# Kernel tuning notes

Measured on AMD Instinct MI355X. Metric: run time of the kernel, lower is better.

The kernel has to match this reference:

```python
import jax, jax.numpy as jnp
import numpy as np

B, L, E = 2, 2048, 1024
NH, DH = 16, 64          # num_heads, attn_hidden_size
HID = 4096               # FFN hidden_size
EPS = 1e-5


def _layernorm(x, g, b):
    mu = jnp.mean(x, axis=-1, keepdims=True)
    var = jnp.var(x, axis=-1, keepdims=True)
    return (x - mu) * jax.lax.rsqrt(var + EPS) * g + b


def setup_inputs() -> dict:
    key = jax.random.key(0)
    ks = jax.random.split(key, 12)
    s = 0.02
    return {
        "x":    jax.random.normal(ks[0], (B, L, E), dtype=jnp.float32),
        "Wa":   jax.random.normal(ks[1], (E, NH * 3 * DH), dtype=jnp.float32) * s,
        "Wout": jax.random.normal(ks[2], (NH * DH, E), dtype=jnp.float32) * s,
        "bout": jnp.zeros((E,), dtype=jnp.float32),
        "W1":   jax.random.normal(ks[3], (E, HID), dtype=jnp.float32) * s,
        "b1":   jnp.zeros((HID,), dtype=jnp.float32),
        "W2":   jax.random.normal(ks[4], (HID, E), dtype=jnp.float32) * s,
        "b2":   jnp.zeros((E,), dtype=jnp.float32),
        "g1":   jnp.ones((E,), dtype=jnp.float32),
        "be1":  jnp.zeros((E,), dtype=jnp.float32),
        "g2":   jnp.ones((E,), dtype=jnp.float32),
        "be2":  jnp.zeros((E,), dtype=jnp.float32),
    }


def _attention(o, Wa, Wout, bout):
    b, l, e = o.shape
    tmp = o @ Wa                                   # (b, l, nh*3*dh)
    tmp = tmp.reshape(b, l, NH, 3 * DH).transpose(0, 2, 1, 3)  # (b, nh, l, 3dh)
    q, k, v = jnp.split(tmp, 3, axis=-1)           # each (b, nh, l, dh)
    scores = jnp.einsum('bhqd,bhkd->bhqk', q, k) / np.sqrt(DH)
    causal = jnp.tril(jnp.ones((l, l), dtype=bool))
    scores = jnp.where(causal, scores, -jnp.inf)
    A = jax.nn.softmax(scores, axis=-1)
    out = jnp.einsum('bhqk,bhkd->bhqd', A, v)      # (b, nh, l, dh)
    out = out.transpose(0, 2, 1, 3).reshape(b, l, NH * DH)
    return out @ Wout + bout


def reference(x, Wa, Wout, bout, W1, b1, W2, b2, g1, be1, g2, be2):
    o = _layernorm(x, g1, be1)
    o = _attention(o, Wa, Wout, bout)
    o = _layernorm(x + o, g2, be2)
    o = o @ W1 + b1          # activation is Identity
    o = x + (o @ W2 + b2)
    return o
```

## Files before the change

### kernel.cpp

```cpp
#include <hip/hip_runtime.h>
#include <hip/hip_bf16.h>

#define BB 2
#define LL 2048
#define EE 1024
#define NHH 16
#define DHH 64
#define HIDD 4096
#define MTOK (BB*LL)
#define NQKV (NHH*3*DHH)

typedef __attribute__((ext_vector_type(8))) short bf16x8;
typedef __attribute__((ext_vector_type(4))) float f32x4;

#define MFMA16(a,b,c) __builtin_amdgcn_mfma_f32_16x16x32_bf16(a,b,c,0,0,0)

static __device__ __forceinline__ void gload_lds16(const void* g, void* lds) {
  __builtin_amdgcn_global_load_lds(
      (const __attribute__((address_space(1))) unsigned int*)g,
      (__attribute__((address_space(3))) unsigned int*)lds, 16, 0, 0);
}

__global__ __launch_bounds__(256)
void convT_kernel(const float* __restrict__ W, __hip_bfloat16* __restrict__ WT,
                  int K, int N) {
  __shared__ float tile[32][33];
  const int tx = threadIdx.x & 31, ty = threadIdx.x >> 5;
  const int n0 = blockIdx.x * 32, k0 = blockIdx.y * 32;
#pragma unroll
  for (int i = 0; i < 4; ++i)
    tile[ty + i*8][tx] = W[(size_t)(k0 + ty + i*8) * N + n0 + tx];
  __syncthreads();
#pragma unroll
  for (int i = 0; i < 4; ++i)
    WT[(size_t)(n0 + ty + i*8) * K + k0 + tx] = __float2bfloat16(tile[tx][ty + i*8]);
}

__global__ __launch_bounds__(256)
void vtrans_kernel(const __hip_bfloat16* __restrict__ qkv,
                   __hip_bfloat16* __restrict__ VT) {
  __shared__ ushort tile[32][34];
  const int tx = threadIdx.x & 31, ty = threadIdx.x >> 5;
  const int tok0 = blockIdx.x * 32;
  const int dh0  = blockIdx.y * 32;
  const int bh   = blockIdx.z;
  const int b = bh >> 4, h = bh & 15;
  const ushort* src = (const ushort*)qkv;
#pragma unroll
  for (int i = 0; i < 4; ++i)
    tile[ty + i*8][tx] =
      src[(size_t)(b*LL + tok0 + ty + i*8) * NQKV + h*192 + 128 + dh0 + tx];
  __syncthreads();
  ushort* dst = (ushort*)VT;
#pragma unroll
  for (int i = 0; i < 4; ++i)
    dst[(size_t)(bh*DHH + dh0 + ty + i*8) * LL + tok0 + tx] = tile[tx][ty + i*8];
}

__global__ __launch_bounds__(256)
void ln_kernel(const float* __restrict__ in, const float* __restrict__ g,
               const float* __restrict__ be, __hip_bfloat16* __restrict__ out) {
  const int row = blockIdx.x;
  const int t = threadIdx.x;
  const float4 v = ((const float4*)(in + (size_t)row * EE))[t];
  float s = v.x + v.y + v.z + v.w;
  float q = v.x*v.x + v.y*v.y + v.z*v.z + v.w*v.w;
#pragma unroll
  for (int off = 32; off >= 1; off >>= 1) {
    s += __shfl_xor(s, off);
    q += __shfl_xor(q, off);
  }
  __shared__ float ps[4], pq[4];
  if ((t & 63) == 0) { ps[t >> 6] = s; pq[t >> 6] = q; }
  __syncthreads();
  s = ps[0] + ps[1] + ps[2] + ps[3];
  q = pq[0] + pq[1] + pq[2] + pq[3];
  const float mean = s * (1.0f / EE);
  const float rstd = rsqrtf(q * (1.0f / EE) - mean * mean + 1e-5f);
  const float4 gg = ((const float4*)g)[t];
  const float4 bb = ((const float4*)be)[t];
  union { ushort4 u; __hip_bfloat16 h[4]; } o;
  o.h[0] = __float2bfloat16((v.x - mean) * rstd * gg.x + bb.x);
  o.h[1] = __float2bfloat16((v.y - mean) * rstd * gg.y + bb.y);
  o.h[2] = __float2bfloat16((v.z - mean) * rstd * gg.z + bb.z);
  o.h[3] = __float2bfloat16((v.w - mean) * rstd * gg.w + bb.w);
  ((ushort4*)(out + (size_t)row * EE))[t] = o.u;
}

template<int BN, int OUT_BF16, int HAS_BIAS, int HAS_RES>
__device__ __forceinline__ void gemm_body(
    const __hip_bfloat16* __restrict__ A, const __hip_bfloat16* __restrict__ BT,
    void* __restrict__ Cv, const float* __restrict__ bias,
    const float* __restrict__ res, int M, int N, int K, int lda, int ldb) {
  constexpr int NF = BN / 32;
  __shared__ alignas(16) __hip_bfloat16 sA[2][128 * 32];
  __shared__ alignas(16) __hip_bfloat16 sB[2][BN * 32];
  const int t = threadIdx.x;
  const int wv = t >> 6, l = t & 63;
  const int lr = l & 15, lk = (l >> 4) * 8;

  const int nwg = gridDim.x * gridDim.y;
  int wg = blockIdx.y * gridDim.x + blockIdx.x;
  wg = (wg & 7) * (nwg >> 3) + (wg >> 3);
  const int bx = wg % gridDim.x, by = wg / gridDim.x;
  const int m0 = by * 128, n0 = bx * BN;

  const int wrow = (wv >> 1) * 64;
  const int wcol = (wv & 1) * (BN / 2);
  const int srow = t >> 2, scol = (t & 3) * 8;
  const __hip_bfloat16* gA = A + (size_t)(m0 + srow) * lda + scol;
  const __hip_bfloat16* gB = BT + (size_t)(n0 + srow) * ldb + scol;

  auto stage = [&](int buf, int k0) {
    char* dA = (char*)(&sA[buf][0]) + wv * 1024;
    gload_lds16(gA + k0, dA);
    gload_lds16(gA + (size_t)64 * lda + k0, dA + 4096);
    char* dB = (char*)(&sB[buf][0]) + wv * 1024;
    gload_lds16(gB + k0, dB);
    if constexpr (BN == 128)
      gload_lds16(gB + (size_t)64 * ldb + k0, dB + 4096);
  };

  f32x4 acc[4][NF] = {};

  auto compute = [&](int buf) {
    bf16x8 af[4], bfv[NF];
#pragma unroll
    for (int mi = 0; mi < 4; ++mi)
      af[mi] = *(const bf16x8*)(&sA[buf][(wrow + mi * 16 + lr) * 32 + lk]);
#pragma unroll
    for (int ni = 0; ni < NF; ++ni)
      bfv[ni] = *(const bf16x8*)(&sB[buf][(wcol + ni * 16 + lr) * 32 + lk]);
#pragma unroll
    for (int mi = 0; mi < 4; ++mi)
#pragma unroll
      for (int ni = 0; ni < NF; ++ni)
        acc[mi][ni] = MFMA16(af[mi], bfv[ni], acc[mi][ni]);
  };

  stage(0, 0);
  __syncthreads();
  for (int k0 = 0; k0 < K; k0 += 64) {
    stage(1, k0 + 32);
    compute(0);
    __syncthreads();
    if (k0 + 64 < K) stage(0, k0 + 64);
    compute(1);
    __syncthreads();
  }

  const int rbase = (l >> 4) * 4;
#pragma unroll
  for (int mi = 0; mi < 4; ++mi) {
#pragma unroll
    for (int ni = 0; ni < NF; ++ni) {
#pragma unroll
      for (int r = 0; r < 4; ++r) {
        const int row = m0 + wrow + mi * 16 + rbase + r;
        const int col = n0 + wcol + ni * 16 + lr;
        float v = acc[mi][ni][r];
        if constexpr (HAS_BIAS) v += bias[col];
        if constexpr (HAS_RES)  v += res[(size_t)row * N + col];
        if constexpr (OUT_BF16)
          ((__hip_bfloat16*)Cv)[(size_t)row * N + col] = __float2bfloat16(v);
        else
          ((float*)Cv)[(size_t)row * N + col] = v;
      }
    }
  }
}

__global__ __launch_bounds__(256)
void gemm_qkv(const __hip_bfloat16* A, const __hip_bfloat16* BT, __hip_bfloat16* C) {
  gemm_body<128,1,0,0>(A, BT, C, nullptr, nullptr, MTOK, NQKV, EE, EE, EE);
}
__global__ __launch_bounds__(256)
void gemm_wout(const __hip_bfloat16* A, const __hip_bfloat16* BT, float* C,
               const float* bias, const float* res) {
  gemm_body<128,0,1,1>(A, BT, C, bias, res, MTOK, EE, EE, EE, EE);
}
__global__ __launch_bounds__(256)
void gemm_ffn1(const __hip_bfloat16* A, const __hip_bfloat16* BT, __hip_bfloat16* C,
               const float* bias) {
  gemm_body<128,1,1,0>(A, BT, C, bias, nullptr, MTOK, HIDD, EE, EE, EE);
}
__global__ __launch_bounds__(256)
void gemm_ffn2p(const __hip_bfloat16* A, const __hip_bfloat16* BT,
                float* P0, float* P1) {
  const int ks = blockIdx.z;
  float* P = ks ? P1 : P0;
  gemm_body<64,0,0,0>(A + ks * 2048, BT + ks * 2048, P, nullptr, nullptr,
                      MTOK, EE, 2048, HIDD, HIDD);
}

__global__ __launch_bounds__(256)
void ffn2_reduce(const float4* __restrict__ P0, const float4* __restrict__ P1,
                 const float4* __restrict__ x, const float* __restrict__ b2,
                 float4* __restrict__ out) {
  const int n4 = MTOK * EE / 4;
  for (int i = blockIdx.x * 256 + threadIdx.x; i < n4; i += 2048 * 256) {
    const float4 b = ((const float4*)b2)[i & 255];
    const float4 p = P0[i], q = P1[i], xx = x[i];
    float4 o;
    o.x = xx.x + b.x + p.x + q.x;
    o.y = xx.y + b.y + p.y + q.y;
    o.z = xx.z + b.z + p.z + q.z;
    o.w = xx.w + b.w + p.w + q.w;
    out[i] = o;
  }
}

__global__ __launch_bounds__(256)
void attn_kernel(const __hip_bfloat16* __restrict__ qkv,
                 const __hip_bfloat16* __restrict__ VT,
                 __hip_bfloat16* __restrict__ out) {
  __shared__ alignas(16) __hip_bfloat16 sP[4][16 * 72];
  const int t = threadIdx.x;
  const int wv = t >> 6, l = t & 63;
  const int lr = l & 15, lg = l >> 4, lk = lg * 8;
  const int hh = blockIdx.y, b = blockIdx.z;
  int qx = blockIdx.x;
  if (b == 1) qx = 31 - qx;
  const int qw = qx * 64 + wv * 16;
  const size_t rowbase = (size_t)b * LL;
  const int hoff = hh * (3 * DHH);
  const __hip_bfloat16* vt = VT + (size_t)((b * NHH + hh) * DHH) * LL;

  bf16x8 qa0, qa1;
  {
    const __hip_bfloat16* qp = qkv + (rowbase + qw + lr) * NQKV + hoff;
    qa0 = *(const bf16x8*)(qp + lk);
    qa1 = *(const bf16x8*)(qp + 32 + lk);
  }

  f32x4 o[4] = {};
  float mrun = -INFINITY, lrun = 0.f;
  __hip_bfloat16* sp = sP[wv];
  const __hip_bfloat16* kbase = qkv + rowbase * NQKV + hoff + DHH;
  const int nt = (qw + 79) >> 6;

  for (int kt = 0; kt < nt; ++kt) {
    const int t0 = kt * 64;
    bf16x8 vb[4][2];
#pragma unroll
    for (int ni = 0; ni < 4; ++ni)
#pragma unroll
      for (int ks = 0; ks < 2; ++ks)
        vb[ni][ks] = *(const bf16x8*)(vt + (size_t)(ni*16 + lr) * LL + t0 + ks*32 + lk);

    f32x4 st[4];
    __builtin_amdgcn_s_setprio(1);
#pragma unroll
    for (int tg = 0; tg < 4; ++tg) {
      const __hip_bfloat16* kp = kbase + (size_t)(t0 + tg*16 + lr) * NQKV;
      bf16x8 kb0 = *(const bf16x8*)(kp + lk);
      bf16x8 kb1 = *(const bf16x8*)(kp + 32 + lk);
      f32x4 z = {0.f, 0.f, 0.f, 0.f};
      z = MFMA16(kb0, qa0, z);
      z = MFMA16(kb1, qa1, z);
      st[tg] = z;
    }
    __builtin_amdgcn_s_setprio(0);

    const bool edge = (kt == nt - 1);
    float tmax = -INFINITY;
#pragma unroll
    for (int tg = 0; tg < 4; ++tg)
#pragma unroll
      for (int r = 0; r < 4; ++r) {
        float v = st[tg][r] * 0.125f;
        if (edge && (t0 + tg*16 + lg*4 + r > qw + lr)) v = -INFINITY;
        st[tg][r] = v;
        tmax = fmaxf(tmax, v);
      }
    tmax = fmaxf(tmax, __shfl_xor(tmax, 16));
    tmax = fmaxf(tmax, __shfl_xor(tmax, 32));
    const float mnew = fmaxf(mrun, tmax);
    const float corr = __expf(mrun - mnew);
    float rs = 0.f;
#pragma unroll
    for (int tg = 0; tg < 4; ++tg) {
      const float p0 = __expf(st[tg][0] - mnew);
      const float p1 = __expf(st[tg][1] - mnew);
      const float p2 = __expf(st[tg][2] - mnew);
      const float p3 = __expf(st[tg][3] - mnew);
      rs += (p0 + p1) + (p2 + p3);
      union { ushort4 u; __hip_bfloat16 h[4]; } pk;
      pk.h[0] = __float2bfloat16(p0);
      pk.h[1] = __float2bfloat16(p1);
      pk.h[2] = __float2bfloat16(p2);
      pk.h[3] = __float2bfloat16(p3);
      *(ushort4*)(sp + lr*72 + tg*16 + lg*4) = pk.u;
    }
    rs += __shfl_xor(rs, 16);
    rs += __shfl_xor(rs, 32);
    lrun = lrun * corr + rs;
    mrun = mnew;

    float corr_o[4];
#pragma unroll
    for (int r = 0; r < 4; ++r)
      corr_o[r] = __shfl(corr, lg*20 + r);
#pragma unroll
    for (int ni = 0; ni < 4; ++ni)
#pragma unroll
      for (int r = 0; r < 4; ++r) o[ni][r] *= corr_o[r];

    bf16x8 pf0 = *(const bf16x8*)(sp + lr*72 + lk);
    bf16x8 pf1 = *(const bf16x8*)(sp + lr*72 + 32 + lk);
    __builtin_amdgcn_s_setprio(1);
#pragma unroll
    for (int ni = 0; ni < 4; ++ni) {
      o[ni] = MFMA16(pf0, vb[ni][0], o[ni]);
      o[ni] = MFMA16(pf1, vb[ni][1], o[ni]);
    }
    __builtin_amdgcn_s_setprio(0);
  }

  float linv[4];
#pragma unroll
  for (int r = 0; r < 4; ++r)
    linv[r] = 1.0f / __shfl(lrun, lg*20 + r);
#pragma unroll
  for (int r = 0; r < 4; ++r) {
    const int qr = qw + lg*4 + r;
    __hip_bfloat16* op = out + (rowbase + qr) * (NHH * DHH) + hh * DHH;
#pragma unroll
    for (int ni = 0; ni < 4; ++ni)
      op[ni*16 + lr] = __float2bfloat16(o[ni][r] * linv[r]);
  }
}

extern "C" void kernel_launch(void* const* d_in, const int* in_sizes, int n_in,
                              void* d_out, int out_size, void* d_ws, size_t ws_size,
                              hipStream_t stream) {
  (void)in_sizes; (void)n_in; (void)out_size; (void)ws_size;
  const float* x    = (const float*)d_in[0];
  const float* Wa   = (const float*)d_in[1];
  const float* Wout = (const float*)d_in[2];
  const float* bout = (const float*)d_in[3];
  const float* W1   = (const float*)d_in[4];
  const float* b1   = (const float*)d_in[5];
  const float* W2   = (const float*)d_in[6];
  const float* b2   = (const float*)d_in[7];
  const float* g1   = (const float*)d_in[8];
  const float* be1  = (const float*)d_in[9];
  const float* g2   = (const float*)d_in[10];
  const float* be2  = (const float*)d_in[11];

  char* ws = (char*)d_ws;
  __hip_bfloat16* WaT   = (__hip_bfloat16*)(ws + 0);
  __hip_bfloat16* WoutT = (__hip_bfloat16*)(ws + 6291456);
  __hip_bfloat16* W1T   = (__hip_bfloat16*)(ws + 8388608);
  __hip_bfloat16* W2T   = (__hip_bfloat16*)(ws + 16777216);
  __hip_bfloat16* o1    = (__hip_bfloat16*)(ws + 25165824);
  __hip_bfloat16* qkv   = (__hip_bfloat16*)(ws + 33554432);
  __hip_bfloat16* VT    = (__hip_bfloat16*)(ws + 58720256);
  __hip_bfloat16* attnb = (__hip_bfloat16*)(ws + 67108864);
  float*          ybuf  = (float*)(ws + 33554432);
  __hip_bfloat16* ln2b  = (__hip_bfloat16*)(ws + 25165824);
  __hip_bfloat16* hbuf  = (__hip_bfloat16*)(ws + 50331648);
  float*          P0    = (float*)(ws + 0);
  float*          P1    = (float*)(ws + 33554432);

  convT_kernel<<<dim3(NQKV/32, EE/32), 256, 0, stream>>>(Wa, WaT, EE, NQKV);
  convT_kernel<<<dim3(EE/32, EE/32), 256, 0, stream>>>(Wout, WoutT, EE, EE);
  convT_kernel<<<dim3(HIDD/32, EE/32), 256, 0, stream>>>(W1, W1T, EE, HIDD);
  convT_kernel<<<dim3(EE/32, HIDD/32), 256, 0, stream>>>(W2, W2T, HIDD, EE);
  ln_kernel<<<MTOK, 256, 0, stream>>>(x, g1, be1, o1);
  gemm_qkv<<<dim3(NQKV/128, MTOK/128), 256, 0, stream>>>(o1, WaT, qkv);
  vtrans_kernel<<<dim3(LL/32, DHH/32, BB*NHH), 256, 0, stream>>>(qkv, VT);
  attn_kernel<<<dim3(LL/64, NHH, BB), 256, 0, stream>>>(qkv, VT, attnb);
  gemm_wout<<<dim3(EE/128, MTOK/128), 256, 0, stream>>>(attnb, WoutT, ybuf, bout, x);
  ln_kernel<<<MTOK, 256, 0, stream>>>(ybuf, g2, be2, ln2b);
  gemm_ffn1<<<dim3(HIDD/128, MTOK/128), 256, 0, stream>>>(ln2b, W1T, hbuf, b1);
  gemm_ffn2p<<<dim3(EE/64, MTOK/128, 2), 256, 0, stream>>>(hbuf, W2T, P0, P1);
  ffn2_reduce<<<2048, 256, 0, stream>>>((const float4*)P0, (const float4*)P1,
                                        (const float4*)x, b2, (float4*)d_out);
}
```

Baseline: 442.9 us.

## Process two query groups per wave in attention and remap blocks across XCDs

Each wave now handles 32 query rows instead of 16, so every K and V fragment loaded from global memory feeds twice as many MFMAs, and the grid is halved to 128-row query tiles. The block index is also remapped so each XCD gets a fixed set of (batch, head) pairs, with query tiles paired long/short to balance causal work, aiming for better L2 reuse of K/V. In exchange, register pressure rises and the block count drops to 512, which can hurt occupancy and load balance. The shuffle index for the per-row correction also changes from lg*20+r to lg*4+r.

```diff
diff --git a/kernel.cpp b/kernel.cpp
--- a/kernel.cpp
+++ b/kernel.cpp
@@ -214,30 +214,37 @@
 void attn_kernel(const __hip_bfloat16* __restrict__ qkv,
                  const __hip_bfloat16* __restrict__ VT,
                  __hip_bfloat16* __restrict__ out) {
-  __shared__ alignas(16) __hip_bfloat16 sP[4][16 * 72];
+  __shared__ alignas(16) __hip_bfloat16 sP[4][32 * 72];
   const int t = threadIdx.x;
   const int wv = t >> 6, l = t & 63;
   const int lr = l & 15, lg = l >> 4, lk = lg * 8;
-  const int hh = blockIdx.y, b = blockIdx.z;
-  int qx = blockIdx.x;
-  if (b == 1) qx = 31 - qx;
-  const int qw = qx * 64 + wv * 16;
+
+  const int f = blockIdx.z * (gridDim.y * gridDim.x)
+              + blockIdx.y * gridDim.x + blockIdx.x;
+  const int xcd = f & 7, s = f >> 3;
+  const int bh = xcd * 4 + (s & 3);
+  const int i = s >> 2;
+  const int qt = (i < 8) ? i : 23 - i;
+  const int b = bh >> 4, hh = bh & 15;
+  const int qw = qt * 128 + wv * 32;
+
   const size_t rowbase = (size_t)b * LL;
   const int hoff = hh * (3 * DHH);
   const __hip_bfloat16* vt = VT + (size_t)((b * NHH + hh) * DHH) * LL;
 
-  bf16x8 qa0, qa1;
-  {
-    const __hip_bfloat16* qp = qkv + (rowbase + qw + lr) * NQKV + hoff;
-    qa0 = *(const bf16x8*)(qp + lk);
-    qa1 = *(const bf16x8*)(qp + 32 + lk);
-  }
-
-  f32x4 o[4] = {};
-  float mrun = -INFINITY, lrun = 0.f;
+  bf16x8 qa[2][2];
+#pragma unroll
+  for (int qg = 0; qg < 2; ++qg)
+#pragma unroll
+    for (int h = 0; h < 2; ++h)
+      qa[qg][h] = *(const bf16x8*)(qkv + (rowbase + qw + qg*16 + lr) * NQKV
+                                   + hoff + h*32 + lk);
+
+  f32x4 o[2][4] = {};
+  float mrun[2] = {-INFINITY, -INFINITY}, lrun[2] = {0.f, 0.f};
   __hip_bfloat16* sp = sP[wv];
   const __hip_bfloat16* kbase = qkv + rowbase * NQKV + hoff + DHH;
-  const int nt = (qw + 79) >> 6;
+  const int nt = (qw >> 6) + 1;
 
   for (int kt = 0; kt < nt; ++kt) {
     const int t0 = kt * 64;
@@ -248,87 +255,100 @@
       for (int ks = 0; ks < 2; ++ks)
         vb[ni][ks] = *(const bf16x8*)(vt + (size_t)(ni*16 + lr) * LL + t0 + ks*32 + lk);
 
-    f32x4 st[4];
+    f32x4 st[2][4];
     __builtin_amdgcn_s_setprio(1);
 #pragma unroll
     for (int tg = 0; tg < 4; ++tg) {
       const __hip_bfloat16* kp = kbase + (size_t)(t0 + tg*16 + lr) * NQKV;
       bf16x8 kb0 = *(const bf16x8*)(kp + lk);
       bf16x8 kb1 = *(const bf16x8*)(kp + 32 + lk);
-      f32x4 z = {0.f, 0.f, 0.f, 0.f};
-      z = MFMA16(kb0, qa0, z);
-      z = MFMA16(kb1, qa1, z);
-      st[tg] = z;
+#pragma unroll
+      for (int qg = 0; qg < 2; ++qg) {
+        f32x4 z = {0.f, 0.f, 0.f, 0.f};
+        z = MFMA16(kb0, qa[qg][0], z);
+        z = MFMA16(kb1, qa[qg][1], z);
+        st[qg][tg] = z;
+      }
     }
     __builtin_amdgcn_s_setprio(0);
 
     const bool edge = (kt == nt - 1);
-    float tmax = -INFINITY;
-#pragma unroll
-    for (int tg = 0; tg < 4; ++tg)
+    float corrv[2];
+#pragma unroll
+    for (int qg = 0; qg < 2; ++qg) {
+      const int q = qw + qg*16 + lr;
+      float tmax = -INFINITY;
+#pragma unroll
+      for (int tg = 0; tg < 4; ++tg)
+#pragma unroll
+        for (int r = 0; r < 4; ++r) {
+          float v = st[qg][tg][r] * 0.125f;
+          if (edge && (t0 + tg*16 + lg*4 + r > q)) v = -INFINITY;
+          st[qg][tg][r] = v;
+          tmax = fmaxf(tmax, v);
+        }
+      tmax = fmaxf(tmax, __shfl_xor(tmax, 16));
+      tmax = fmaxf(tmax, __shfl_xor(tmax, 32));
+      const float mnew = fmaxf(mrun[qg], tmax);
+      corrv[qg] = __expf(mrun[qg] - mnew);
+      float rs = 0.f;
+#pragma unroll
+      for (int tg = 0; tg < 4; ++tg) {
+        const float p0 = __expf(st[qg][tg][0] - mnew);
+        const float p1 = __expf(st[qg][tg][1] - mnew);
+        const float p2 = __expf(st[qg][tg][2] - mnew);
+        const float p3 = __expf(st[qg][tg][3] - mnew);
+        rs += (p0 + p1) + (p2 + p3);
+        union { ushort4 u; __hip_bfloat16 h[4]; } pk;
+        pk.h[0] = __float2bfloat16(p0);
+        pk.h[1] = __float2bfloat16(p1);
+        pk.h[2] = __float2bfloat16(p2);
+        pk.h[3] = __float2bfloat16(p3);
+        *(ushort4*)(sp + (qg*16 + lr)*72 + tg*16 + lg*4) = pk.u;
+      }
+      rs += __shfl_xor(rs, 16);
+      rs += __shfl_xor(rs, 32);
+      lrun[qg] = lrun[qg] * corrv[qg] + rs;
+      mrun[qg] = mnew;
+    }
+
+#pragma unroll
+    for (int qg = 0; qg < 2; ++qg)
 #pragma unroll
       for (int r = 0; r < 4; ++r) {
-        float v = st[tg][r] * 0.125f;
-        if (edge && (t0 + tg*16 + lg*4 + r > qw + lr)) v = -INFINITY;
-        st[tg][r] = v;
-        tmax = fmaxf(tmax, v);
+        const float c = __shfl(corrv[qg], lg*4 + r);
+#pragma unroll
+        for (int ni = 0; ni < 4; ++ni) o[qg][ni][r] *= c;
       }
-    tmax = fmaxf(tmax, __shfl_xor(tmax, 16));
-    tmax = fmaxf(tmax, __shfl_xor(tmax, 32));
-    const float mnew = fmaxf(mrun, tmax);
-    const float corr = __expf(mrun - mnew);
-    float rs = 0.f;
-#pragma unroll
-    for (int tg = 0; tg < 4; ++tg) {
-      const float p0 = __expf(st[tg][0] - mnew);
-      const float p1 = __expf(st[tg][1] - mnew);
-      const float p2 = __expf(st[tg][2] - mnew);
-      const float p3 = __expf(st[tg][3] - mnew);
-      rs += (p0 + p1) + (p2 + p3);
-      union { ushort4 u; __hip_bfloat16 h[4]; } pk;
-      pk.h[0] = __float2bfloat16(p0);
-      pk.h[1] = __float2bfloat16(p1);
-      pk.h[2] = __float2bfloat16(p2);
-      pk.h[3] = __float2bfloat16(p3);
-      *(ushort4*)(sp + lr*72 + tg*16 + lg*4) = pk.u;
-    }
-    rs += __shfl_xor(rs, 16);
-    rs += __shfl_xor(rs, 32);
-    lrun = lrun * corr + rs;
-    mrun = mnew;
-
-    float corr_o[4];
-#pragma unroll
-    for (int r = 0; r < 4; ++r)
-      corr_o[r] = __shfl(corr, lg*20 + r);
-#pragma unroll
-    for (int ni = 0; ni < 4; ++ni)
-#pragma unroll
-      for (int r = 0; r < 4; ++r) o[ni][r] *= corr_o[r];
-
-    bf16x8 pf0 = *(const bf16x8*)(sp + lr*72 + lk);
-    bf16x8 pf1 = *(const bf16x8*)(sp + lr*72 + 32 + lk);
+
+    bf16x8 pf[2][2];
+#pragma unroll
+    for (int qg = 0; qg < 2; ++qg)
+#pragma unroll
+      for (int ks = 0; ks < 2; ++ks)
+        pf[qg][ks] = *(const bf16x8*)(sp + (qg*16 + lr)*72 + ks*32 + lk);
     __builtin_amdgcn_s_setprio(1);
 #pragma unroll
-    for (int ni = 0; ni < 4; ++ni) {
-      o[ni] = MFMA16(pf0, vb[ni][0], o[ni]);
-      o[ni] = MFMA16(pf1, vb[ni][1], o[ni]);
-    }
+    for (int qg = 0; qg < 2; ++qg)
+#pragma unroll
+      for (int ni = 0; ni < 4; ++ni) {
+        o[qg][ni] = MFMA16(pf[qg][0], vb[ni][0], o[qg][ni]);
+        o[qg][ni] = MFMA16(pf[qg][1], vb[ni][1], o[qg][ni]);
+      }
     __builtin_amdgcn_s_setprio(0);
   }
 
-  float linv[4];
-#pragma unroll
-  for (int r = 0; r < 4; ++r)
-    linv[r] = 1.0f / __shfl(lrun, lg*20 + r);
-#pragma unroll
-  for (int r = 0; r < 4; ++r) {
-    const int qr = qw + lg*4 + r;
-    __hip_bfloat16* op = out + (rowbase + qr) * (NHH * DHH) + hh * DHH;
-#pragma unroll
-    for (int ni = 0; ni < 4; ++ni)
-      op[ni*16 + lr] = __float2bfloat16(o[ni][r] * linv[r]);
-  }
+#pragma unroll
+  for (int qg = 0; qg < 2; ++qg)
+#pragma unroll
+    for (int r = 0; r < 4; ++r) {
+      const float linv = 1.0f / __shfl(lrun[qg], lg*4 + r);
+      const int qr = qw + qg*16 + lg*4 + r;
+      __hip_bfloat16* op = out + (rowbase + qr) * (NHH * DHH) + hh * DHH;
+#pragma unroll
+      for (int ni = 0; ni < 4; ++ni)
+        op[ni*16 + lr] = __float2bfloat16(o[qg][ni][r] * linv);
+    }
 }
 
 extern "C" void kernel_launch(void* const* d_in, const int* in_sizes, int n_in,
@@ -370,7 +390,7 @@
   ln_kernel<<<MTOK, 256, 0, stream>>>(x, g1, be1, o1);
   gemm_qkv<<<dim3(NQKV/128, MTOK/128), 256, 0, stream>>>(o1, WaT, qkv);
   vtrans_kernel<<<dim3(LL/32, DHH/32, BB*NHH), 256, 0, stream>>>(qkv, VT);
-  attn_kernel<<<dim3(LL/64, NHH, BB), 256, 0, stream>>>(qkv, VT, attnb);
+  attn_kernel<<<dim3(LL/128, NHH, BB), 256, 0, stream>>>(qkv, VT, attnb);
   gemm_wout<<<dim3(EE/128, MTOK/128), 256, 0, stream>>>(attnb, WoutT, ybuf, bout, x);
   ln_kernel<<<MTOK, 256, 0, stream>>>(ybuf, g2, be2, ln2b);
   gemm_ffn1<<<dim3(HIDD/128, MTOK/128), 256, 0, stream>>>(ln2b, W1T, hbuf, b1);
```

Result: faster. 416.7 us (-5.9%).
